# Performance work log

Measured on AMD Instinct MI355X. Metric: run time of the kernel, lower is better.

## Reference

```python
import jax, jax.numpy as jnp
import numpy as np
from jax import lax


def setup_inputs() -> dict:
    key = jax.random.key(0)
    ks = jax.random.split(key, 3)
    N, Cin, Cout, H, W = 4, 256, 256, 96, 96
    x = jax.random.normal(ks[0], (N, Cin, H, W), jnp.float32)
    # DCNv2-style internal offset/mask conv: 27 = 9 dy + 9 dx + 9 mask logits
    w_off = jax.random.normal(ks[1], (27, Cin, 3, 3), jnp.float32) * 0.01
    b_off = jnp.zeros((27,), jnp.float32)
    w = jax.random.normal(ks[2], (Cout, Cin, 3, 3), jnp.float32) * (1.0 / np.sqrt(Cin * 9))
    b = jnp.zeros((Cout,), jnp.float32)
    gamma = jnp.ones((Cout,), jnp.float32)
    beta = jnp.zeros((Cout,), jnp.float32)
    return {"x": x, "w_off": w_off, "b_off": b_off, "w": w, "b": b, "gamma": gamma, "beta": beta}


def _bilinear(img, py, px):
    # img: [C,H,W]; py,px: [K,H,W] float sampling coords. Zero outside bounds.
    C, H, W = img.shape
    flat = img.reshape(C, -1)
    y0 = jnp.floor(py)
    x0 = jnp.floor(px)
    ly = py - y0
    lx = px - x0

    def gather(yc, xc):
        valid = (yc >= 0) & (yc <= H - 1) & (xc >= 0) & (xc <= W - 1)
        yi = jnp.clip(yc, 0, H - 1).astype(jnp.int32)
        xi = jnp.clip(xc, 0, W - 1).astype(jnp.int32)
        idx = (yi * W + xi).reshape(-1)
        v = flat[:, idx].reshape((C,) + yc.shape)  # [C,K,H,W]
        return v * valid.astype(img.dtype)

    v00 = gather(y0, x0)
    v01 = gather(y0, x0 + 1)
    v10 = gather(y0 + 1, x0)
    v11 = gather(y0 + 1, x0 + 1)
    return (v00 * (1 - ly) * (1 - lx) + v01 * (1 - ly) * lx
            + v10 * ly * (1 - lx) + v11 * ly * lx)


def _forward(x, w_off, b_off, w, b, gamma, beta):
    N, C, H, W = x.shape
    Cout = w.shape[0]
    dn = ("NCHW", "OIHW", "NCHW")
    # internal offset/mask conv (3x3, stride 1, pad 1)
    om = lax.conv_general_dilated(x, w_off, (1, 1), [(1, 1), (1, 1)], dimension_numbers=dn)
    om = om + b_off[None, :, None, None]
    dy, dx, m = om[:, :9], om[:, 9:18], jax.nn.sigmoid(om[:, 18:])
    # base 3x3 kernel grid, dilation 1, padding 1 (centered taps -1..1)
    ky, kx = jnp.meshgrid(jnp.arange(3) - 1, jnp.arange(3) - 1, indexing="ij")
    py = dy + jnp.arange(H, dtype=x.dtype)[None, None, :, None] + ky.reshape(1, 9, 1, 1).astype(x.dtype)
    px = dx + jnp.arange(W, dtype=x.dtype)[None, None, None, :] + kx.reshape(1, 9, 1, 1).astype(x.dtype)
    sampled = jax.vmap(_bilinear)(x, py, px)  # [N,C,9,H,W]
    sampled = sampled * m[:, None]            # DCNv2 modulation mask
    y = jnp.einsum("nckhw,ock->nohw", sampled, w.reshape(Cout, C, 9))
    y = y + b[None, :, None, None]
    # BatchNorm2d (training-mode batch statistics) + ReLU
    mean = y.mean(axis=(0, 2, 3))
    var = y.var(axis=(0, 2, 3))
    y = (y - mean[None, :, None, None]) * lax.rsqrt(var[None, :, None, None] + 1e-5)
    y = y * gamma[None, :, None, None] + beta[None, :, None, None]
    return jax.nn.relu(y)


def reference(x, w_off, b_off, w, b, gamma, beta):
    return _forward(x, w_off, b_off, w, b, gamma, beta)
```

## Files before the change

kernel.cpp:

```cpp
#include <hip/hip_runtime.h>
#include <cmath>

#define H 96
#define W 96
#define HW 9216
#define CIN 256
#define COUT 256
#define NB 4
#define NCH 72
#define NGR 36

typedef float f32x4 __attribute__((ext_vector_type(4)));
typedef short bf16x8 __attribute__((ext_vector_type(8)));

__device__ __forceinline__ unsigned short f2bf(float f) {
  unsigned int u = __float_as_uint(f);
  u += 0x7fff + ((u >> 16) & 1);
  return (unsigned short)(u >> 16);
}
__device__ __forceinline__ float bf2f(unsigned short u) {
  return __uint_as_float(((unsigned int)u) << 16);
}
__device__ __forceinline__ float bfLo(unsigned int u) {
  return __uint_as_float(u << 16);
}
__device__ __forceinline__ float bfHi(unsigned int u) {
  return __uint_as_float(u & 0xffff0000u);
}

__global__ __launch_bounds__(256)
void xt_convert(const float* __restrict__ x, unsigned short* __restrict__ xT) {
  __shared__ unsigned short ls[64][72];
  int tid = threadIdx.x;
  int hwbase = blockIdx.x * 64;
  int cbase  = blockIdx.y * 64;
  int n      = blockIdx.z;

  {
    int cl = tid >> 2, qd = tid & 3;
    const float* src = x + ((size_t)(n * CIN + cbase + cl)) * HW + hwbase + qd * 16;
#pragma unroll
    for (int m = 0; m < 4; ++m) {
      float4 v = *(const float4*)(src + m * 4);
      int hwl = qd * 16 + m * 4;
      ls[hwl + 0][cl] = f2bf(v.x);
      ls[hwl + 1][cl] = f2bf(v.y);
      ls[hwl + 2][cl] = f2bf(v.z);
      ls[hwl + 3][cl] = f2bf(v.w);
    }
  }
  __syncthreads();
  {
    int hw = tid >> 2, part = tid & 3;
    unsigned short* dst = xT + ((size_t)(n * HW + hwbase + hw)) * CIN + cbase + part * 16;
    *(uint4*)(dst + 0) = *(const uint4*)(&ls[hw][part * 16 + 0]);
    *(uint4*)(dst + 8) = *(const uint4*)(&ls[hw][part * 16 + 8]);
  }
}

__global__ __launch_bounds__(256)
void wa_convert(const float* __restrict__ w, unsigned short* __restrict__ Ag) {
  int gid = blockIdx.x * 256 + threadIdx.x;
  int ch = gid >> 10;
  int rest = gid & 1023;
  int ot = rest >> 6, l = rest & 63;
  int o = ot * 16 + (l & 15);
  int k = ch >> 3, cc = ch & 7;
  int cbase = cc * 32 + (l >> 4) * 8;
  unsigned short r[8];
#pragma unroll
  for (int j = 0; j < 8; ++j)
    r[j] = f2bf(w[((size_t)o * CIN + cbase + j) * 9 + k]);
  uint4 pk;
  pk.x = (unsigned int)r[0] | ((unsigned int)r[1] << 16);
  pk.y = (unsigned int)r[2] | ((unsigned int)r[3] << 16);
  pk.z = (unsigned int)r[4] | ((unsigned int)r[5] << 16);
  pk.w = (unsigned int)r[6] | ((unsigned int)r[7] << 16);
  *(uint4*)(Ag + (size_t)gid * 8) = pk;
}

__global__ __launch_bounds__(256)
void wa2_convert(const float* __restrict__ w_off, unsigned short* __restrict__ Ag2) {
  int gid = blockIdx.x * 256 + threadIdx.x;
  int ch = gid >> 7;
  int rest = gid & 127;
  int ot = rest >> 6, l = rest & 63;
  int o = ot * 16 + (l & 15);
  int k = ch >> 3, cc = ch & 7;
  int cbase = cc * 32 + (l >> 4) * 8;
  unsigned short r[8];
#pragma unroll
  for (int j = 0; j < 8; ++j)
    r[j] = (o < 27) ? f2bf(w_off[((size_t)o * CIN + cbase + j) * 9 + k]) : (unsigned short)0;
  uint4 pk;
  pk.x = (unsigned int)r[0] | ((unsigned int)r[1] << 16);
  pk.y = (unsigned int)r[2] | ((unsigned int)r[3] << 16);
  pk.z = (unsigned int)r[4] | ((unsigned int)r[5] << 16);
  pk.w = (unsigned int)r[6] | ((unsigned int)r[7] << 16);
  *(uint4*)(Ag2 + (size_t)gid * 8) = pk;
}

__global__ __launch_bounds__(256)
void offset_gemm(const unsigned short* __restrict__ xT,
                 const unsigned short* __restrict__ Ag2,
                 const float* __restrict__ b_off,
                 float* __restrict__ py, float* __restrict__ px,
                 float* __restrict__ mk) {
  __shared__ int sPos[9][64];
  __shared__ unsigned short sB[2][4096];

  int tid = threadIdx.x;
  int wv = tid >> 6, lane = tid & 63, quad = lane >> 4, l16 = lane & 15;
  int pixBase = blockIdx.x * 64;
  int n = blockIdx.y;
  const unsigned short* xTn = xT + (size_t)n * HW * CIN;

  if (tid < 64) {
    int hwp = pixBase + tid;
    int hh = hwp / W, wx = hwp % W;
#pragma unroll
    for (int ty = 0; ty < 3; ++ty) {
#pragma unroll
      for (int tx = 0; tx < 3; ++tx) {
        int iy = hh + ty - 1, ix = wx + tx - 1;
        bool ok = (iy >= 0) && (iy < H) && (ix >= 0) && (ix < W);
        sPos[ty * 3 + tx][tid] = ok ? (iy * W + ix) : -1;
      }
    }
  }
  __syncthreads();

  int pix0 = tid >> 3, ck0 = tid & 7;
  int pix1 = 32 + (tid >> 3), ck1 = ck0;
  int a0 = (ck0 >> 2) * 2048 + (pix0 >> 4) * 512 + ((ck0 & 3) * 16 + ((pix0 & 15) ^ (ck0 & 3))) * 8;
  int a1 = (ck1 >> 2) * 2048 + (pix1 >> 4) * 512 + ((ck1 & 3) * 16 + ((pix1 & 15) ^ (ck1 & 3))) * 8;

  f32x4 acc[2];
  acc[0] = (f32x4){0.f, 0.f, 0.f, 0.f};
  acc[1] = (f32x4){0.f, 0.f, 0.f, 0.f};

  uint4 d0, d1;
  auto sload = [&](int k, int cc2) {
    int p0 = sPos[k][pix0], p1 = sPos[k][pix1];
    d0 = (uint4){0, 0, 0, 0};
    d1 = (uint4){0, 0, 0, 0};
    if (p0 >= 0) d0 = *(const uint4*)(xTn + (size_t)p0 * CIN + cc2 * 64 + ck0 * 8);
    if (p1 >= 0) d1 = *(const uint4*)(xTn + (size_t)p1 * CIN + cc2 * 64 + ck1 * 8);
  };

  bf16x8 afr[4], afrn[4];
  auto aload = [&](int k, int cc2, bf16x8* dst) {
    int ch = k * 8 + cc2 * 2;
#pragma unroll
    for (int s = 0; s < 2; ++s)
#pragma unroll
      for (int ot = 0; ot < 2; ++ot)
        dst[s * 2 + ot] = *(const bf16x8*)(Ag2 + ((size_t)((ch + s) * 2 + ot) * 64 + lane) * 8);
  };

  sload(0, 0);
  aload(0, 0, afr);
  *(uint4*)(&sB[0][a0]) = d0;
  *(uint4*)(&sB[0][a1]) = d1;
  __syncthreads();

  int rdAddr0 = wv * 512 + (quad * 16 + (l16 ^ quad)) * 8;

  int kC = 0, ccC = 0;
  for (int g = 0; g < NGR; ++g) {
    int p = g & 1;
    int kN = kC + 1, ccN = ccC;
    if (kN == 9) { kN = 0; ccN = ccC + 1; }
    if (g < NGR - 1) {
      sload(kN, ccN);
      aload(kN, ccN, afrn);
    }

#pragma unroll
    for (int s = 0; s < 2; ++s) {
      bf16x8 bfr = *(const bf16x8*)(&sB[p][s * 2048 + rdAddr0]);
      acc[0] = __builtin_amdgcn_mfma_f32_16x16x32_bf16(afr[s * 2 + 0], bfr, acc[0], 0, 0, 0);
      acc[1] = __builtin_amdgcn_mfma_f32_16x16x32_bf16(afr[s * 2 + 1], bfr, acc[1], 0, 0, 0);
    }

    if (g < NGR - 1) {
      *(uint4*)(&sB[1 - p][a0]) = d0;
      *(uint4*)(&sB[1 - p][a1]) = d1;
      __syncthreads();
#pragma unroll
      for (int i = 0; i < 4; ++i) afr[i] = afrn[i];
      kC = kN; ccC = ccN;
    }
  }

  int pix = pixBase + wv * 16 + l16;
  int he = pix / W, we = pix % W;
#pragma unroll
  for (int ot = 0; ot < 2; ++ot) {
#pragma unroll
    for (int r = 0; r < 4; ++r) {
      int kk = ot * 16 + quad * 4 + r;
      if (kk >= 27) continue;
      float v = acc[ot][r] + b_off[kk];
      if (kk < 9) {
        py[(size_t)(n * 9 + kk) * HW + pix] = v + (float)he + (float)(kk / 3 - 1);
      } else if (kk < 18) {
        int j = kk - 9;
        px[(size_t)(n * 9 + j) * HW + pix] = v + (float)we + (float)(j % 3 - 1);
      } else {
        mk[(size_t)(n * 9 + (kk - 18)) * HW + pix] = 1.f / (1.f + expf(-v));
      }
    }
  }
}

__global__ __launch_bounds__(512)
void fused_gemm(const unsigned short* __restrict__ xT,
                const unsigned short* __restrict__ Ag,
                const float* __restrict__ py,
                const float* __restrict__ px,
                const float* __restrict__ mk,
                unsigned short* __restrict__ yb,
                float* __restrict__ sumArr, float* __restrict__ sqArr) {
  __shared__ int   sIdx[9][4][64];
  __shared__ float sWgt[9][4][64];
  __shared__ unsigned short sB[2][4096];

  int tid = threadIdx.x;
  int wv = tid >> 6, lane = tid & 63, quad = lane >> 4, l16 = lane & 15;
  int pixBase = blockIdx.x * 64;
  int n = blockIdx.y;
  const unsigned short* xTn = xT + (size_t)n * HW * CIN;

  {
    int pix0 = tid & 63;
    int k0 = tid >> 6;
#pragma unroll
    for (int rep = 0; rep < 2; ++rep) {
      int k = (rep == 0) ? k0 : 8;
      if (rep == 1 && tid >= 64) break;
      int off = (n * 9 + k) * HW + pixBase + pix0;
      float fy = py[off], fx = px[off], fm = mk[off];
      float y0f = floorf(fy), x0f = floorf(fx);
      float ly = fy - y0f, lx = fx - x0f;
      int y0 = (int)y0f, x0 = (int)x0f;
      int cy0 = min(max(y0, 0), H - 1), cy1 = min(max(y0 + 1, 0), H - 1);
      int cx0 = min(max(x0, 0), W - 1), cx1 = min(max(x0 + 1, 0), W - 1);
      float vy0 = (y0 >= 0 && y0 <= H - 1) ? 1.f : 0.f;
      float vy1 = (y0 + 1 >= 0 && y0 + 1 <= H - 1) ? 1.f : 0.f;
      float vx0 = (x0 >= 0 && x0 <= W - 1) ? 1.f : 0.f;
      float vx1 = (x0 + 1 >= 0 && x0 + 1 <= W - 1) ? 1.f : 0.f;
      sIdx[k][0][pix0] = cy0 * W + cx0;
      sIdx[k][1][pix0] = cy0 * W + cx1;
      sIdx[k][2][pix0] = cy1 * W + cx0;
      sIdx[k][3][pix0] = cy1 * W + cx1;
      sWgt[k][0][pix0] = (1.f - ly) * (1.f - lx) * fm * vy0 * vx0;
      sWgt[k][1][pix0] = (1.f - ly) * lx * fm * vy0 * vx1;
      sWgt[k][2][pix0] = ly * (1.f - lx) * fm * vy1 * vx0;
      sWgt[k][3][pix0] = ly * lx * fm * vy1 * vx1;
    }
  }
  __syncthreads();

  int pixS  = ((wv & 3) << 4) | (lane >> 2);
  int qS    = lane & 3;
  int chunk = ((wv >> 2) << 2) | qS;
  int co    = chunk * 8;
  int sAddr = (chunk >> 2) * 2048 + (wv & 3) * 512 +
              ((qS << 4) | ((lane >> 2) & 15) ^ (qS & 0)) * 8;
  sAddr = (chunk >> 2) * 2048 + (wv & 3) * 512 + (qS * 16 + ((lane >> 2) ^ qS)) * 8;

  f32x4 acc[2][4];
#pragma unroll
  for (int i = 0; i < 2; ++i)
#pragma unroll
    for (int pt = 0; pt < 4; ++pt) acc[i][pt] = (f32x4){0.f, 0.f, 0.f, 0.f};

  int i0, i1, i2, i3;
  float w0, w1, w2, w3;
  auto loadTap = [&](int k) {
    i0 = sIdx[k][0][pixS]; i1 = sIdx[k][1][pixS];
    i2 = sIdx[k][2][pixS]; i3 = sIdx[k][3][pixS];
    w0 = sWgt[k][0][pixS]; w1 = sWgt[k][1][pixS];
    w2 = sWgt[k][2][pixS]; w3 = sWgt[k][3][pixS];
  };

  uint4 cn[4];
  auto sload = [&](int cc2) {
    int coff = cc2 * 64 + co;
    cn[0] = *(const uint4*)(xTn + (size_t)i0 * CIN + coff);
    cn[1] = *(const uint4*)(xTn + (size_t)i1 * CIN + coff);
    cn[2] = *(const uint4*)(xTn + (size_t)i2 * CIN + coff);
    cn[3] = *(const uint4*)(xTn + (size_t)i3 * CIN + coff);
  };
  auto blend8 = [&]() -> uint4 {
    const unsigned int* u0 = (const unsigned int*)&cn[0];
    const unsigned int* u1 = (const unsigned int*)&cn[1];
    const unsigned int* u2 = (const unsigned int*)&cn[2];
    const unsigned int* u3 = (const unsigned int*)&cn[3];
    unsigned int r[4];
#pragma unroll
    for (int p = 0; p < 4; ++p) {
      float lo = bfLo(u0[p]) * w0;
      lo = fmaf(bfLo(u1[p]), w1, lo);
      lo = fmaf(bfLo(u2[p]), w2, lo);
      lo = fmaf(bfLo(u3[p]), w3, lo);
      float hi = bfHi(u0[p]) * w0;
      hi = fmaf(bfHi(u1[p]), w1, hi);
      hi = fmaf(bfHi(u2[p]), w2, hi);
      hi = fmaf(bfHi(u3[p]), w3, hi);
      r[p] = (unsigned int)f2bf(lo) | ((unsigned int)f2bf(hi) << 16);
    }
    return (uint4){r[0], r[1], r[2], r[3]};
  };

  bf16x8 afr[4], afrn[4];
  auto aload = [&](int k, int cc2, bf16x8* dst) {
    int ch = k * 8 + cc2 * 2;
#pragma unroll
    for (int s = 0; s < 2; ++s)
#pragma unroll
      for (int ot = 0; ot < 2; ++ot)
        dst[s * 2 + ot] = *(const bf16x8*)(Ag + ((size_t)((ch + s) * 16 + 2 * wv + ot) * 64 + lane) * 8);
  };

  loadTap(0);
  sload(0);
  aload(0, 0, afr);
  {
    uint4 b = blend8();
    *(uint4*)(&sB[0][sAddr]) = b;
  }
  __syncthreads();

  int rdBase = (quad * 16 + (l16 ^ quad)) * 8;

  int kC = 0, ccC = 0;
  for (int g = 0; g < NGR; ++g) {
    int p = g & 1;
    int kN = kC + 1, ccN = ccC;
    if (kN == 9) { kN = 0; ccN = ccC + 1; }
    if (g < NGR - 1) {
      loadTap(kN);
      sload(ccN);
      aload(kN, ccN, afrn);
    }

#pragma unroll
    for (int s = 0; s < 2; ++s) {
      bf16x8 bfr[4];
#pragma unroll
      for (int pt = 0; pt < 4; ++pt)
        bfr[pt] = *(const bf16x8*)(&sB[p][s * 2048 + pt * 512 + rdBase]);
#pragma unroll
      for (int pt = 0; pt < 4; ++pt) {
        acc[0][pt] = __builtin_amdgcn_mfma_f32_16x16x32_bf16(afr[s * 2 + 0], bfr[pt], acc[0][pt], 0, 0, 0);
        acc[1][pt] = __builtin_amdgcn_mfma_f32_16x16x32_bf16(afr[s * 2 + 1], bfr[pt], acc[1][pt], 0, 0, 0);
      }
    }

    if (g < NGR - 1) {
      uint4 b = blend8();
      *(uint4*)(&sB[1 - p][sAddr]) = b;
      __syncthreads();
#pragma unroll
      for (int i = 0; i < 4; ++i) afr[i] = afrn[i];
      kC = kN; ccC = ccN;
    }
  }

#pragma unroll
  for (int ot = 0; ot < 2; ++ot) {
#pragma unroll
    for (int r = 0; r < 4; ++r) {
      int o = (2 * wv + ot) * 16 + quad * 4 + r;
      unsigned short* rowp = yb + (size_t)(n * COUT + o) * HW + pixBase;
      float s = 0.f, q = 0.f;
#pragma unroll
      for (int pt = 0; pt < 4; ++pt) {
        float v = acc[ot][pt][r];
        rowp[pt * 16 + l16] = f2bf(v);
        s += v;
        q = fmaf(v, v, q);
      }
#pragma unroll
      for (int m = 8; m >= 1; m >>= 1) {
        s += __shfl_xor(s, m, 64);
        q += __shfl_xor(q, m, 64);
      }
      if (l16 == 0) {
        atomicAdd(&sumArr[o], s);
        atomicAdd(&sqArr[o], q);
      }
    }
  }
}

__global__ __launch_bounds__(256)
void bn_finalize(const float* __restrict__ sumArr, const float* __restrict__ sqArr,
                 const float* __restrict__ gamma, const float* __restrict__ beta,
                 float* __restrict__ scaleArr, float* __restrict__ shiftArr) {
  int o = threadIdx.x;
  const float inv = 1.f / (float)(NB * HW);
  float mean = sumArr[o] * inv;
  float var = sqArr[o] * inv - mean * mean;
  float sc = rsqrtf(var + 1e-5f) * gamma[o];
  scaleArr[o] = sc;
  shiftArr[o] = beta[o] - mean * sc;
}

__global__ __launch_bounds__(256)
void bn_apply(const unsigned short* __restrict__ yb,
              float* __restrict__ out,
              const float* __restrict__ scaleArr,
              const float* __restrict__ shiftArr) {
  int gid = blockIdx.x * 256 + threadIdx.x;
  int base = gid * 8;
  int o = (base / HW) % COUT;
  float scale = scaleArr[o], shift = shiftArr[o];
  uint4 v = ((const uint4*)yb)[gid];
  float4 a, b;
  a.x = fmaxf(fmaf(bf2f((unsigned short)(v.x & 0xffff)), scale, shift), 0.f);
  a.y = fmaxf(fmaf(bf2f((unsigned short)(v.x >> 16)), scale, shift), 0.f);
  a.z = fmaxf(fmaf(bf2f((unsigned short)(v.y & 0xffff)), scale, shift), 0.f);
  a.w = fmaxf(fmaf(bf2f((unsigned short)(v.y >> 16)), scale, shift), 0.f);
  b.x = fmaxf(fmaf(bf2f((unsigned short)(v.z & 0xffff)), scale, shift), 0.f);
  b.y = fmaxf(fmaf(bf2f((unsigned short)(v.z >> 16)), scale, shift), 0.f);
  b.z = fmaxf(fmaf(bf2f((unsigned short)(v.w & 0xffff)), scale, shift), 0.f);
  b.w = fmaxf(fmaf(bf2f((unsigned short)(v.w >> 16)), scale, shift), 0.f);
  *(float4*)&out[base] = a;
  *(float4*)&out[base + 4] = b;
}

extern "C" void kernel_launch(void* const* d_in, const int* in_sizes, int n_in,
                              void* d_out, int out_size, void* d_ws, size_t ws_size,
                              hipStream_t stream) {
  const float* x     = (const float*)d_in[0];
  const float* w_off = (const float*)d_in[1];
  const float* b_off = (const float*)d_in[2];
  const float* w     = (const float*)d_in[3];
  const float* gamma = (const float*)d_in[5];
  const float* beta  = (const float*)d_in[6];
  float* out = (float*)d_out;

  float* ws = (float*)d_ws;
  float* py = ws;
  float* px = py + 331776;
  float* mk = px + 331776;
  unsigned short* Ag  = (unsigned short*)(mk + 331776);
  unsigned short* Ag2 = Ag + 589824;
  float* sumArr   = (float*)(Ag2 + 73728);
  float* sqArr    = sumArr + 256;
  float* scaleArr = sqArr + 256;
  float* shiftArr = scaleArr + 256;
  unsigned short* yb = (unsigned short*)(shiftArr + 256);
  unsigned short* xT = yb + 9437184;

  hipMemsetAsync(sumArr, 0, 512 * sizeof(float), stream);

  dim3 gT(HW / 64, CIN / 64, NB);
  xt_convert<<<gT, 256, 0, stream>>>(x, xT);

  wa_convert<<<(NCH * 16 * 64) / 256, 256, 0, stream>>>(w, Ag);
  wa2_convert<<<(NCH * 2 * 64) / 256, 256, 0, stream>>>(w_off, Ag2);

  dim3 gO(HW / 64, NB);
  offset_gemm<<<gO, 256, 0, stream>>>(xT, Ag2, b_off, py, px, mk);

  dim3 gG(HW / 64, NB);
  fused_gemm<<<gG, 512, 0, stream>>>(xT, Ag, py, px, mk, yb, sumArr, sqArr);

  bn_finalize<<<1, 256, 0, stream>>>(sumArr, sqArr, gamma, beta, scaleArr, shiftArr);
  bn_apply<<<(NB * COUT * HW / 8) / 256, 256, 0, stream>>>(yb, out, scaleArr, shiftArr);
}
```

Baseline: 281.3 us.

## Deepen gather prefetch to two stages in offset and deformable GEMM loops

Restructures the main loops of offset_gemm and fused_gemm so that global gathers for step g+2 are issued before the MFMA phase of step g, using two ping-pong register sets. This gives more latency hiding for the scattered bilinear loads. It also adds min-blocks-per-CU hints to launch_bounds and vectorises the bf16 bilinear blend with float2 math. The cost is higher register pressure: the extra buffered loads may conflict with the occupancy hint and cause spills.

```diff
diff --git a/kernel.cpp b/kernel.cpp
--- a/kernel.cpp
+++ b/kernel.cpp
@@ -11,6 +11,7 @@
 #define NGR 36
 
 typedef float f32x4 __attribute__((ext_vector_type(4)));
+typedef float f32x2 __attribute__((ext_vector_type(2)));
 typedef short bf16x8 __attribute__((ext_vector_type(8)));
 
 __device__ __forceinline__ unsigned short f2bf(float f) {
@@ -21,11 +22,11 @@
 __device__ __forceinline__ float bf2f(unsigned short u) {
   return __uint_as_float(((unsigned int)u) << 16);
 }
-__device__ __forceinline__ float bfLo(unsigned int u) {
-  return __uint_as_float(u << 16);
-}
-__device__ __forceinline__ float bfHi(unsigned int u) {
-  return __uint_as_float(u & 0xffff0000u);
+__device__ __forceinline__ f32x2 up2(unsigned int u) {
+  f32x2 r;
+  r.x = __uint_as_float(u << 16);
+  r.y = __uint_as_float(u & 0xffff0000u);
+  return r;
 }
 
 __global__ __launch_bounds__(256)
@@ -100,7 +101,7 @@
   *(uint4*)(Ag2 + (size_t)gid * 8) = pk;
 }
 
-__global__ __launch_bounds__(256)
+__global__ __launch_bounds__(256, 4)
 void offset_gemm(const unsigned short* __restrict__ xT,
                  const unsigned short* __restrict__ Ag2,
                  const float* __restrict__ b_off,
@@ -131,26 +132,28 @@
   __syncthreads();
 
   int pix0 = tid >> 3, ck0 = tid & 7;
-  int pix1 = 32 + (tid >> 3), ck1 = ck0;
+  int pix1 = 32 + (tid >> 3);
   int a0 = (ck0 >> 2) * 2048 + (pix0 >> 4) * 512 + ((ck0 & 3) * 16 + ((pix0 & 15) ^ (ck0 & 3))) * 8;
-  int a1 = (ck1 >> 2) * 2048 + (pix1 >> 4) * 512 + ((ck1 & 3) * 16 + ((pix1 & 15) ^ (ck1 & 3))) * 8;
+  int a1 = (ck0 >> 2) * 2048 + (pix1 >> 4) * 512 + ((ck0 & 3) * 16 + ((pix1 & 15) ^ (ck0 & 3))) * 8;
 
   f32x4 acc[2];
   acc[0] = (f32x4){0.f, 0.f, 0.f, 0.f};
   acc[1] = (f32x4){0.f, 0.f, 0.f, 0.f};
 
-  uint4 d0, d1;
-  auto sload = [&](int k, int cc2) {
+  uint4 dA[2], dB[2];
+  auto issue = [&](int g, uint4* d) {
+    int k = g % 9, c2 = g / 9;
     int p0 = sPos[k][pix0], p1 = sPos[k][pix1];
-    d0 = (uint4){0, 0, 0, 0};
-    d1 = (uint4){0, 0, 0, 0};
-    if (p0 >= 0) d0 = *(const uint4*)(xTn + (size_t)p0 * CIN + cc2 * 64 + ck0 * 8);
-    if (p1 >= 0) d1 = *(const uint4*)(xTn + (size_t)p1 * CIN + cc2 * 64 + ck1 * 8);
-  };
-
-  bf16x8 afr[4], afrn[4];
-  auto aload = [&](int k, int cc2, bf16x8* dst) {
-    int ch = k * 8 + cc2 * 2;
+    d[0] = (uint4){0, 0, 0, 0};
+    d[1] = (uint4){0, 0, 0, 0};
+    if (p0 >= 0) d[0] = *(const uint4*)(xTn + (size_t)p0 * CIN + c2 * 64 + ck0 * 8);
+    if (p1 >= 0) d[1] = *(const uint4*)(xTn + (size_t)p1 * CIN + c2 * 64 + ck0 * 8);
+  };
+
+  bf16x8 afrA[4], afrB[4];
+  auto aload = [&](int g, bf16x8* dst) {
+    int k = g % 9, c2 = g / 9;
+    int ch = k * 8 + c2 * 2;
 #pragma unroll
     for (int s = 0; s < 2; ++s)
 #pragma unroll
@@ -158,38 +161,39 @@
         dst[s * 2 + ot] = *(const bf16x8*)(Ag2 + ((size_t)((ch + s) * 2 + ot) * 64 + lane) * 8);
   };
 
-  sload(0, 0);
-  aload(0, 0, afr);
-  *(uint4*)(&sB[0][a0]) = d0;
-  *(uint4*)(&sB[0][a1]) = d1;
-  __syncthreads();
-
   int rdAddr0 = wv * 512 + (quad * 16 + (l16 ^ quad)) * 8;
-
-  int kC = 0, ccC = 0;
-  for (int g = 0; g < NGR; ++g) {
-    int p = g & 1;
-    int kN = kC + 1, ccN = ccC;
-    if (kN == 9) { kN = 0; ccN = ccC + 1; }
-    if (g < NGR - 1) {
-      sload(kN, ccN);
-      aload(kN, ccN, afrn);
-    }
-
+  auto mfmaPhase = [&](int buf, bf16x8* afr) {
 #pragma unroll
     for (int s = 0; s < 2; ++s) {
-      bf16x8 bfr = *(const bf16x8*)(&sB[p][s * 2048 + rdAddr0]);
+      bf16x8 bfr = *(const bf16x8*)(&sB[buf][s * 2048 + rdAddr0]);
       acc[0] = __builtin_amdgcn_mfma_f32_16x16x32_bf16(afr[s * 2 + 0], bfr, acc[0], 0, 0, 0);
       acc[1] = __builtin_amdgcn_mfma_f32_16x16x32_bf16(afr[s * 2 + 1], bfr, acc[1], 0, 0, 0);
     }
-
-    if (g < NGR - 1) {
-      *(uint4*)(&sB[1 - p][a0]) = d0;
-      *(uint4*)(&sB[1 - p][a1]) = d1;
+  };
+  auto store = [&](uint4* d, int buf) {
+    *(uint4*)(&sB[buf][a0]) = d[0];
+    *(uint4*)(&sB[buf][a1]) = d[1];
+  };
+
+  issue(0, dA);
+  aload(0, afrA);
+  store(dA, 0);
+  issue(1, dB);
+  __syncthreads();
+
+  for (int g = 0; g < NGR; g += 2) {
+    if (g + 2 < NGR) issue(g + 2, dA);
+    aload(g + 1, afrB);
+    mfmaPhase(0, afrA);
+    store(dB, 1);
+    __syncthreads();
+
+    if (g + 3 < NGR) issue(g + 3, dB);
+    if (g + 2 < NGR) aload(g + 2, afrA);
+    mfmaPhase(1, afrB);
+    if (g + 2 < NGR) {
+      store(dA, 0);
       __syncthreads();
-#pragma unroll
-      for (int i = 0; i < 4; ++i) afr[i] = afrn[i];
-      kC = kN; ccC = ccN;
     }
   }
 
@@ -214,7 +218,7 @@
   }
 }
 
-__global__ __launch_bounds__(512)
+__global__ __launch_bounds__(512, 4)
 void fused_gemm(const unsigned short* __restrict__ xT,
                 const unsigned short* __restrict__ Ag,
                 const float* __restrict__ py,
@@ -266,9 +270,7 @@
   int qS    = lane & 3;
   int chunk = ((wv >> 2) << 2) | qS;
   int co    = chunk * 8;
-  int sAddr = (chunk >> 2) * 2048 + (wv & 3) * 512 +
-              ((qS << 4) | ((lane >> 2) & 15) ^ (qS & 0)) * 8;
-  sAddr = (chunk >> 2) * 2048 + (wv & 3) * 512 + (qS * 16 + ((lane >> 2) ^ qS)) * 8;
+  int sAddr = (chunk >> 2) * 2048 + (wv & 3) * 512 + (qS * 16 + ((lane >> 2) ^ qS)) * 8;
 
   f32x4 acc[2][4];
 #pragma unroll
@@ -276,47 +278,42 @@
 #pragma unroll
     for (int pt = 0; pt < 4; ++pt) acc[i][pt] = (f32x4){0.f, 0.f, 0.f, 0.f};
 
-  int i0, i1, i2, i3;
-  float w0, w1, w2, w3;
-  auto loadTap = [&](int k) {
-    i0 = sIdx[k][0][pixS]; i1 = sIdx[k][1][pixS];
-    i2 = sIdx[k][2][pixS]; i3 = sIdx[k][3][pixS];
-    w0 = sWgt[k][0][pixS]; w1 = sWgt[k][1][pixS];
-    w2 = sWgt[k][2][pixS]; w3 = sWgt[k][3][pixS];
-  };
-
-  uint4 cn[4];
-  auto sload = [&](int cc2) {
-    int coff = cc2 * 64 + co;
+  uint4 cnA[4], cnB[4];
+  float wgA[4], wgB[4];
+  auto issue = [&](int g, uint4* cn, float* wt) {
+    int k = g % 9, c2 = g / 9;
+    int i0 = sIdx[k][0][pixS], i1 = sIdx[k][1][pixS];
+    int i2 = sIdx[k][2][pixS], i3 = sIdx[k][3][pixS];
+    int coff = c2 * 64 + co;
     cn[0] = *(const uint4*)(xTn + (size_t)i0 * CIN + coff);
     cn[1] = *(const uint4*)(xTn + (size_t)i1 * CIN + coff);
     cn[2] = *(const uint4*)(xTn + (size_t)i2 * CIN + coff);
     cn[3] = *(const uint4*)(xTn + (size_t)i3 * CIN + coff);
-  };
-  auto blend8 = [&]() -> uint4 {
-    const unsigned int* u0 = (const unsigned int*)&cn[0];
-    const unsigned int* u1 = (const unsigned int*)&cn[1];
-    const unsigned int* u2 = (const unsigned int*)&cn[2];
-    const unsigned int* u3 = (const unsigned int*)&cn[3];
-    unsigned int r[4];
-#pragma unroll
-    for (int p = 0; p < 4; ++p) {
-      float lo = bfLo(u0[p]) * w0;
-      lo = fmaf(bfLo(u1[p]), w1, lo);
-      lo = fmaf(bfLo(u2[p]), w2, lo);
-      lo = fmaf(bfLo(u3[p]), w3, lo);
-      float hi = bfHi(u0[p]) * w0;
-      hi = fmaf(bfHi(u1[p]), w1, hi);
-      hi = fmaf(bfHi(u2[p]), w2, hi);
-      hi = fmaf(bfHi(u3[p]), w3, hi);
-      r[p] = (unsigned int)f2bf(lo) | ((unsigned int)f2bf(hi) << 16);
-    }
-    return (uint4){r[0], r[1], r[2], r[3]};
-  };
-
-  bf16x8 afr[4], afrn[4];
-  auto aload = [&](int k, int cc2, bf16x8* dst) {
-    int ch = k * 8 + cc2 * 2;
+    wt[0] = sWgt[k][0][pixS]; wt[1] = sWgt[k][1][pixS];
+    wt[2] = sWgt[k][2][pixS]; wt[3] = sWgt[k][3][pixS];
+  };
+
+  auto blendOne = [&](unsigned int u0, unsigned int u1, unsigned int u2,
+                      unsigned int u3, const float* wt) -> unsigned int {
+    f32x2 s = up2(u0) * wt[0];
+    s += up2(u1) * wt[1];
+    s += up2(u2) * wt[2];
+    s += up2(u3) * wt[3];
+    return (unsigned int)f2bf(s.x) | ((unsigned int)f2bf(s.y) << 16);
+  };
+  auto blendStore = [&](uint4* cn, const float* wt, int buf) {
+    uint4 r;
+    r.x = blendOne(cn[0].x, cn[1].x, cn[2].x, cn[3].x, wt);
+    r.y = blendOne(cn[0].y, cn[1].y, cn[2].y, cn[3].y, wt);
+    r.z = blendOne(cn[0].z, cn[1].z, cn[2].z, cn[3].z, wt);
+    r.w = blendOne(cn[0].w, cn[1].w, cn[2].w, cn[3].w, wt);
+    *(uint4*)(&sB[buf][sAddr]) = r;
+  };
+
+  bf16x8 afrA[4], afrB[4];
+  auto aload = [&](int g, bf16x8* dst) {
+    int k = g % 9, c2 = g / 9;
+    int ch = k * 8 + c2 * 2;
 #pragma unroll
     for (int s = 0; s < 2; ++s)
 #pragma unroll
@@ -324,48 +321,41 @@
         dst[s * 2 + ot] = *(const bf16x8*)(Ag + ((size_t)((ch + s) * 16 + 2 * wv + ot) * 64 + lane) * 8);
   };
 
-  loadTap(0);
-  sload(0);
-  aload(0, 0, afr);
-  {
-    uint4 b = blend8();
-    *(uint4*)(&sB[0][sAddr]) = b;
-  }
-  __syncthreads();
-
   int rdBase = (quad * 16 + (l16 ^ quad)) * 8;
-
-  int kC = 0, ccC = 0;
-  for (int g = 0; g < NGR; ++g) {
-    int p = g & 1;
-    int kN = kC + 1, ccN = ccC;
-    if (kN == 9) { kN = 0; ccN = ccC + 1; }
-    if (g < NGR - 1) {
-      loadTap(kN);
-      sload(ccN);
-      aload(kN, ccN, afrn);
-    }
-
+  auto mfmaPhase = [&](int buf, bf16x8* afr) {
 #pragma unroll
     for (int s = 0; s < 2; ++s) {
       bf16x8 bfr[4];
 #pragma unroll
       for (int pt = 0; pt < 4; ++pt)
-        bfr[pt] = *(const bf16x8*)(&sB[p][s * 2048 + pt * 512 + rdBase]);
+        bfr[pt] = *(const bf16x8*)(&sB[buf][s * 2048 + pt * 512 + rdBase]);
 #pragma unroll
       for (int pt = 0; pt < 4; ++pt) {
         acc[0][pt] = __builtin_amdgcn_mfma_f32_16x16x32_bf16(afr[s * 2 + 0], bfr[pt], acc[0][pt], 0, 0, 0);
         acc[1][pt] = __builtin_amdgcn_mfma_f32_16x16x32_bf16(afr[s * 2 + 1], bfr[pt], acc[1][pt], 0, 0, 0);
       }
     }
-
-    if (g < NGR - 1) {
-      uint4 b = blend8();
-      *(uint4*)(&sB[1 - p][sAddr]) = b;
+  };
+
+  issue(0, cnA, wgA);
+  aload(0, afrA);
+  blendStore(cnA, wgA, 0);
+  issue(1, cnB, wgB);
+  __syncthreads();
+
+  for (int g = 0; g < NGR; g += 2) {
+    if (g + 2 < NGR) issue(g + 2, cnA, wgA);
+    aload(g + 1, afrB);
+    mfmaPhase(0, afrA);
+    blendStore(cnB, wgB, 1);
+    __syncthreads();
+
+    if (g + 3 < NGR) issue(g + 3, cnB, wgB);
+    if (g + 2 < NGR) aload(g + 2, afrA);
+    mfmaPhase(1, afrB);
+    if (g + 2 < NGR) {
+      blendStore(cnA, wgA, 0);
       __syncthreads();
-#pragma unroll
-      for (int i = 0; i < 4; ++i) afr[i] = afrn[i];
-      kC = kN; ccC = ccN;
     }
   }
 
```

Result: slower. 327.6 us (+16.5%).
